# Kernel tuning notes

Hardware: AMD Instinct MI355X
Metric: run time of the kernel (lower is better)

## Reference

```python
import jax, jax.numpy as jnp
import numpy as np

DT = 0.1
ROUTER_BLOCKS = 64
REPEAT = 64
IN_SIZE = 2048
HIDDEN = 4096
NNZ_W = int(IN_SIZE * HIDDEN * 0.01)   # 83886
NNZ_R = int(HIDDEN * HIDDEN * 0.01)    # 167772
BATCH = 512


def sparse_linear(x, rows, cols, vals, bias, out_features):
    """Edge-list sparse matmul: out[b, cols[e]] += x[b, rows[e]] * vals[e].
    Equivalent to torch.addmm(bias, x, W_csr) with W built from COO (coalesce
    sums duplicates; scatter-add does the same)."""
    contrib = x[:, rows] * vals  # [B, nnz]
    out = jnp.zeros((x.shape[0], out_features), x.dtype).at[:, cols].add(contrib)
    return out + bias


def setup_inputs() -> dict:
    key = jax.random.key(0)
    ks = jax.random.split(key, 20)
    inp = {}
    inp["x"] = jax.random.normal(ks[0], (BATCH, IN_SIZE), jnp.float32)
    inp["h_prev"] = jax.random.normal(ks[1], (BATCH, HIDDEN), jnp.float32)
    inp["gate"] = jax.random.uniform(ks[2], (BATCH, 1), jnp.float32)
    # SparseLinear params (init scale 1/sqrt(in_features), bias zeros)
    inp["W_vals"] = jax.random.normal(ks[3], (NNZ_W,), jnp.float32) / np.sqrt(IN_SIZE).astype(np.float32)
    inp["W_bias"] = jnp.zeros((HIDDEN,), jnp.float32)
    inp["R_vals"] = jax.random.normal(ks[4], (NNZ_R,), jnp.float32) / np.sqrt(HIDDEN).astype(np.float32)
    inp["R_bias"] = jnp.zeros((HIDDEN,), jnp.float32)
    inp["P_vals"] = jax.random.normal(ks[5], (NNZ_R,), jnp.float32) / np.sqrt(HIDDEN).astype(np.float32)
    inp["P_bias"] = jnp.zeros((HIDDEN,), jnp.float32)
    inp["router_w"] = jax.random.normal(ks[6], (ROUTER_BLOCKS, IN_SIZE), jnp.float32) / np.sqrt(IN_SIZE).astype(np.float32)
    inp["router_b"] = jnp.zeros((ROUTER_BLOCKS,), jnp.float32)
    # tau ~ U(0.1, 0.5) per TAU_CONCEPT_RANGE
    inp["tau"] = jax.random.uniform(ks[7], (HIDDEN,), jnp.float32) * 0.4 + 0.1
    # edge lists (int constants)
    inp["W_rows"] = jax.random.randint(ks[8], (NNZ_W,), 0, IN_SIZE, jnp.int32)
    inp["W_cols"] = jax.random.randint(ks[9], (NNZ_W,), 0, HIDDEN, jnp.int32)
    inp["R_rows"] = jax.random.randint(ks[10], (NNZ_R,), 0, HIDDEN, jnp.int32)
    inp["R_cols"] = jax.random.randint(ks[11], (NNZ_R,), 0, HIDDEN, jnp.int32)
    inp["P_rows"] = jax.random.randint(ks[12], (NNZ_R,), 0, HIDDEN, jnp.int32)
    inp["P_cols"] = jax.random.randint(ks[13], (NNZ_R,), 0, HIDDEN, jnp.int32)
    return inp


def reference(x, h_prev, gate, W_vals, W_bias, R_vals, R_bias, P_vals, P_bias,
              router_w, router_b, tau, W_rows, W_cols, R_rows, R_cols, P_rows, P_cols):
    r_gate = jax.nn.sigmoid(x @ router_w.T + router_b)            # [B, 64]
    mask = jnp.repeat(r_gate, REPEAT, axis=1)[:, :HIDDEN]          # [B, hidden]
    sensory = sparse_linear(x, W_rows, W_cols, W_vals, W_bias, HIDDEN) * mask
    rec = sparse_linear(h_prev, R_rows, R_cols, R_vals, R_bias, HIDDEN)
    target = jnp.tanh(sensory + rec)
    h_new = h_prev + gate * (target - h_prev) * (DT / tau)
    pred = sparse_linear(h_new, P_rows, P_cols, P_vals, P_bias, HIDDEN)
    return (h_new, pred)
```

## Files before the change

### kernel.cpp

```cpp
#include <hip/hip_runtime.h>
#include <math.h>

namespace {

constexpr int B     = 512;
constexpr int IN    = 2048;
constexpr int HID   = 4096;
constexpr int NNZ_W = 83886;
constexpr int NNZ_R = 167772;
constexpr int NTOT  = NNZ_W + 2 * NNZ_R;
constexpr int NCOLS = 3 * HID;
constexpr int SLOT  = 128;
constexpr float DT  = 0.1f;

typedef float f4 __attribute__((ext_vector_type(4)));
typedef float f2 __attribute__((ext_vector_type(2)));

struct ushort4_t { unsigned short x, y, z, w; };

__device__ __forceinline__ float bf2f(unsigned short u) {
  return __uint_as_float((unsigned int)u << 16);
}
__device__ __forceinline__ unsigned short f2bf(float f) {
  unsigned int u = __float_as_uint(f);
  u += 0x7FFFu + ((u >> 16) & 1u);
  return (unsigned short)(u >> 16);
}

__global__ void prep_k(const float* __restrict__ x, unsigned short* __restrict__ xTb,
                       const float* __restrict__ h, float* __restrict__ hT,
                       unsigned short* __restrict__ hTb,
                       const float* __restrict__ rw, const float* __restrict__ rb,
                       float* __restrict__ rgT, int* __restrict__ cnt) {
  __shared__ float sh[4 * IN];
  const int blk = blockIdx.x;
  const int tid = threadIdx.x;

  if (blk < 768) {
    const bool isX = blk < 256;
    const float* src; int C, tb;
    if (isX) { src = x; C = IN;  tb = blk; }
    else     { src = h; C = HID; tb = blk - 256; }
    const int tx_n = C / 64;
    const int bx = (tb % tx_n) * 64;
    const int by = (tb / tx_n) * 64;
    const int tx = tid & 63;
    const int ty = tid >> 6;
    for (int i = ty; i < 64; i += 8)
      sh[i * 65 + tx] = src[(size_t)(by + i) * C + bx + tx];
    __syncthreads();
    for (int i = ty; i < 64; i += 8) {
      const float v = sh[tx * 65 + i];
      const size_t di = (size_t)(bx + i) * B + by + tx;
      if (isX) xTb[di] = f2bf(v);
      else     { hT[di] = v; hTb[di] = f2bf(v); }
    }
  } else if (blk < 896) {
    const int b0 = (blk - 768) * 4;
    for (int k = tid; k < 4 * IN; k += 512) sh[k] = x[(size_t)b0 * IN + k];
    __syncthreads();
    const int wave = tid >> 6;
    const int lane = tid & 63;
#pragma unroll
    for (int j = 0; j < 8; ++j) {
      const int o = wave * 8 + j;
      const float* w = rw + (size_t)o * IN;
      float s0 = 0.f, s1 = 0.f, s2 = 0.f, s3 = 0.f;
      for (int i = 0; i < IN / 64; ++i) {
        const float wv = w[lane + 64 * i];
        s0 += sh[0 * IN + lane + 64 * i] * wv;
        s1 += sh[1 * IN + lane + 64 * i] * wv;
        s2 += sh[2 * IN + lane + 64 * i] * wv;
        s3 += sh[3 * IN + lane + 64 * i] * wv;
      }
#pragma unroll
      for (int d = 1; d < 64; d <<= 1) {
        s0 += __shfl_xor(s0, d);
        s1 += __shfl_xor(s1, d);
        s2 += __shfl_xor(s2, d);
        s3 += __shfl_xor(s3, d);
      }
      if (lane == 0) {
        const float bias = rb[o];
        rgT[o * B + b0 + 0] = 1.f / (1.f + expf(-(s0 + bias)));
        rgT[o * B + b0 + 1] = 1.f / (1.f + expf(-(s1 + bias)));
        rgT[o * B + b0 + 2] = 1.f / (1.f + expf(-(s2 + bias)));
        rgT[o * B + b0 + 3] = 1.f / (1.f + expf(-(s3 + bias)));
      }
    }
  } else {
    const int i = (blk - 896) * 512 + tid;
    if (i < NCOLS) cnt[i] = 0;
  }
}

__global__ void slotscat_k(const int* __restrict__ Wc, const int* __restrict__ Rc,
                           const int* __restrict__ Pc, const int* __restrict__ Wr,
                           const int* __restrict__ Rr, const int* __restrict__ Pr,
                           const float* __restrict__ Wv, const float* __restrict__ Rv,
                           const float* __restrict__ Pv, int* __restrict__ cnt,
                           float2* __restrict__ packed) {
  const int i = blockIdx.x * blockDim.x + threadIdx.x;
  if (i >= NTOT) return;
  int gc, r; float v;
  if (i < NNZ_W)              { gc = Wc[i];                 r = Wr[i]; v = Wv[i]; }
  else if (i < NNZ_W + NNZ_R) { int j = i - NNZ_W;          gc = HID + Rc[j];     r = Rr[j]; v = Rv[j]; }
  else                        { int j = i - NNZ_W - NNZ_R; gc = 2 * HID + Pc[j]; r = Pr[j]; v = Pv[j]; }
  const int p = atomicAdd(&cnt[gc], 1);
  packed[(size_t)gc * SLOT + p] = make_float2(v, __int_as_float(r));
}

__device__ __forceinline__ f4 gather_col_bf(const unsigned short* __restrict__ srcb,
                                            const float2* __restrict__ packed,
                                            int gc, int n, int boff, float bias) {
  f4 acc; acc.x = bias; acc.y = bias; acc.z = bias; acc.w = bias;
  const f2* ep = (const f2*)(packed + (size_t)gc * SLOT);
  int i = 0;
  for (; i + 8 <= n; i += 8) {
    f2 e[8]; ushort4_t s[8];
#pragma unroll
    for (int j = 0; j < 8; ++j) e[j] = ep[i + j];
#pragma unroll
    for (int j = 0; j < 8; ++j)
      s[j] = *(const ushort4_t*)(srcb + (size_t)__float_as_int(e[j].y) * B + boff);
#pragma unroll
    for (int j = 0; j < 8; ++j) {
      acc.x += e[j].x * bf2f(s[j].x);
      acc.y += e[j].x * bf2f(s[j].y);
      acc.z += e[j].x * bf2f(s[j].z);
      acc.w += e[j].x * bf2f(s[j].w);
    }
  }
  for (; i < n; ++i) {
    const f2 e = ep[i];
    const ushort4_t s = *(const ushort4_t*)(srcb + (size_t)__float_as_int(e.y) * B + boff);
    acc.x += e.x * bf2f(s.x);
    acc.y += e.x * bf2f(s.y);
    acc.z += e.x * bf2f(s.z);
    acc.w += e.x * bf2f(s.w);
  }
  return acc;
}

__device__ __forceinline__ void col_chunk(int blk, int wave, int& c, int& boff,
                                          int lane, int& cgrp, int& chunk) {
  const int p = blk & 7;
  chunk = p >> 2;
  cgrp = ((p & 3) << 8) | (blk >> 3);
  c = cgrp * 4 + wave;
  boff = chunk * 256 + lane * 4;
}

__device__ __forceinline__ void store_tile_T(float* __restrict__ tile,
                                             const f4 v, int wave, int lane,
                                             int cgrp, int chunk,
                                             float* __restrict__ out) {
  ((f4*)tile)[wave * 64 + lane] = v;
  __syncthreads();
  const int t = threadIdx.x;
  f4 o;
  o.x = tile[0 * 256 + t];
  o.y = tile[1 * 256 + t];
  o.z = tile[2 * 256 + t];
  o.w = tile[3 * 256 + t];
  *(f4*)(out + (size_t)(chunk * 256 + t) * HID + cgrp * 4) = o;
}

__global__ void fused_gc_k(const unsigned short* __restrict__ xTb,
                           const unsigned short* __restrict__ hTb,
                           const float* __restrict__ hT,
                           const float2* __restrict__ packed, const int* __restrict__ cnt,
                           const float* __restrict__ rgT,
                           const float* __restrict__ gate, const float* __restrict__ tau,
                           const float* __restrict__ wb, const float* __restrict__ rb,
                           float* __restrict__ out_h, unsigned short* __restrict__ hnb) {
  __shared__ float tile[4 * 256];
  int c, boff, cgrp, chunk;
  const int wave = threadIdx.x >> 6, lane = threadIdx.x & 63;
  col_chunk(blockIdx.x, wave, c, boff, lane, cgrp, chunk);

  const f4 sens = gather_col_bf(xTb, packed, c, cnt[c], boff, wb[c]);
  const f4 rec  = gather_col_bf(hTb, packed, HID + c, cnt[HID + c], boff, rb[c]);

  const f4 m  = *(const f4*)(rgT + (size_t)(c >> 6) * B + boff);
  const f4 g  = *(const f4*)(gate + boff);
  const f4 hp = *(const f4*)(hT + (size_t)c * B + boff);
  const float k = DT / tau[c];
  f4 hn;
  hn.x = hp.x + g.x * (tanhf(sens.x * m.x + rec.x) - hp.x) * k;
  hn.y = hp.y + g.y * (tanhf(sens.y * m.y + rec.y) - hp.y) * k;
  hn.z = hp.z + g.z * (tanhf(sens.z * m.z + rec.z) - hp.z) * k;
  hn.w = hp.w + g.w * (tanhf(sens.w * m.w + rec.w) - hp.w) * k;

  ushort4_t hb;
  hb.x = f2bf(hn.x); hb.y = f2bf(hn.y); hb.z = f2bf(hn.z); hb.w = f2bf(hn.w);
  *(ushort4_t*)(hnb + (size_t)c * B + boff) = hb;

  store_tile_T(tile, hn, wave, lane, cgrp, chunk, out_h);
}

__global__ void pred_k(const unsigned short* __restrict__ hnb,
                       const float2* __restrict__ packed, const int* __restrict__ cnt,
                       const float* __restrict__ pb, float* __restrict__ out_p) {
  __shared__ float tile[4 * 256];
  int c, boff, cgrp, chunk;
  const int wave = threadIdx.x >> 6, lane = threadIdx.x & 63;
  col_chunk(blockIdx.x, wave, c, boff, lane, cgrp, chunk);
  const f4 p = gather_col_bf(hnb, packed, 2 * HID + c, cnt[2 * HID + c], boff, pb[c]);
  store_tile_T(tile, p, wave, lane, cgrp, chunk, out_p);
}

}

extern "C" void kernel_launch(void* const* d_in, const int* in_sizes, int n_in,
                              void* d_out, int out_size, void* d_ws, size_t ws_size,
                              hipStream_t stream) {
  const float* x        = (const float*)d_in[0];
  const float* h_prev   = (const float*)d_in[1];
  const float* gate     = (const float*)d_in[2];
  const float* W_vals   = (const float*)d_in[3];
  const float* W_bias   = (const float*)d_in[4];
  const float* R_vals   = (const float*)d_in[5];
  const float* R_bias   = (const float*)d_in[6];
  const float* P_vals   = (const float*)d_in[7];
  const float* P_bias   = (const float*)d_in[8];
  const float* router_w = (const float*)d_in[9];
  const float* router_b = (const float*)d_in[10];
  const float* tau      = (const float*)d_in[11];
  const int* W_rows = (const int*)d_in[12];
  const int* W_cols = (const int*)d_in[13];
  const int* R_rows = (const int*)d_in[14];
  const int* R_cols = (const int*)d_in[15];
  const int* P_rows = (const int*)d_in[16];
  const int* P_cols = (const int*)d_in[17];

  float* ws = (float*)d_ws;
  unsigned short* xTb = (unsigned short*)ws;
  float*  hT     = ws + (size_t)IN * B / 2;
  unsigned short* hTb = (unsigned short*)(hT + (size_t)HID * B);
  float*  rgT    = (float*)(hTb + (size_t)HID * B);
  unsigned short* hnb = (unsigned short*)(rgT + 64 * B);
  float2* packed = (float2*)(hnb + (size_t)HID * B);
  int*    cnt    = (int*)(packed + (size_t)NCOLS * SLOT);

  float* out_h = (float*)d_out;
  float* out_p = out_h + (size_t)B * HID;

  prep_k<<<920, 512, 0, stream>>>(x, xTb, h_prev, hT, hTb,
                                  router_w, router_b, rgT, cnt);

  slotscat_k<<<(NTOT + 255) / 256, 256, 0, stream>>>(W_cols, R_cols, P_cols,
                                                     W_rows, R_rows, P_rows,
                                                     W_vals, R_vals, P_vals,
                                                     cnt, packed);

  fused_gc_k<<<2048, 256, 0, stream>>>(xTb, hTb, hT, packed, cnt, rgT,
                                       gate, tau, W_bias, R_bias, out_h, hnb);

  pred_k<<<2048, 256, 0, stream>>>(hnb, packed, cnt, P_bias, out_p);
}
```

Before: 111.9 us.

## Have each wave cover the full batch with 8-wide bf16 gathers per lane

Each lane now processes 8 batch elements instead of 4, loading 16-byte bf16 vectors per gathered row. Each block covers four columns across the whole batch, which halves the block count and removes the batch-chunk swizzle. Every edge-list entry is now read once per column instead of once per batch chunk, which cuts redundant packed-edge loads and index latency. In exchange, register pressure rises, the shared tile doubles, and fewer blocks are available to hide gather latency.

```diff
diff --git a/kernel.cpp b/kernel.cpp
--- a/kernel.cpp
+++ b/kernel.cpp
@@ -15,8 +15,9 @@
 
 typedef float f4 __attribute__((ext_vector_type(4)));
 typedef float f2 __attribute__((ext_vector_type(2)));
-
-struct ushort4_t { unsigned short x, y, z, w; };
+typedef unsigned short us8 __attribute__((ext_vector_type(8)));
+
+struct f8 { f4 lo, hi; };
 
 __device__ __forceinline__ float bf2f(unsigned short u) {
   return __uint_as_float((unsigned int)u << 16);
@@ -110,60 +111,59 @@
   packed[(size_t)gc * SLOT + p] = make_float2(v, __int_as_float(r));
 }
 
-__device__ __forceinline__ f4 gather_col_bf(const unsigned short* __restrict__ srcb,
-                                            const float2* __restrict__ packed,
-                                            int gc, int n, int boff, float bias) {
-  f4 acc; acc.x = bias; acc.y = bias; acc.z = bias; acc.w = bias;
+__device__ __forceinline__ f8 gather_col_bf8(const unsigned short* __restrict__ srcb,
+                                             const float2* __restrict__ packed,
+                                             int gc, int n, int boff, float bias) {
+  f4 a0; a0.x = bias; a0.y = bias; a0.z = bias; a0.w = bias;
+  f4 a1 = a0;
   const f2* ep = (const f2*)(packed + (size_t)gc * SLOT);
   int i = 0;
   for (; i + 8 <= n; i += 8) {
-    f2 e[8]; ushort4_t s[8];
+    f2 e[8]; us8 s[8];
 #pragma unroll
     for (int j = 0; j < 8; ++j) e[j] = ep[i + j];
 #pragma unroll
     for (int j = 0; j < 8; ++j)
-      s[j] = *(const ushort4_t*)(srcb + (size_t)__float_as_int(e[j].y) * B + boff);
+      s[j] = *(const us8*)(srcb + (size_t)__float_as_int(e[j].y) * B + boff);
 #pragma unroll
     for (int j = 0; j < 8; ++j) {
-      acc.x += e[j].x * bf2f(s[j].x);
-      acc.y += e[j].x * bf2f(s[j].y);
-      acc.z += e[j].x * bf2f(s[j].z);
-      acc.w += e[j].x * bf2f(s[j].w);
+      const float v = e[j].x;
+      a0.x += v * bf2f(s[j][0]); a0.y += v * bf2f(s[j][1]);
+      a0.z += v * bf2f(s[j][2]); a0.w += v * bf2f(s[j][3]);
+      a1.x += v * bf2f(s[j][4]); a1.y += v * bf2f(s[j][5]);
+      a1.z += v * bf2f(s[j][6]); a1.w += v * bf2f(s[j][7]);
     }
   }
   for (; i < n; ++i) {
     const f2 e = ep[i];
-    const ushort4_t s = *(const ushort4_t*)(srcb + (size_t)__float_as_int(e.y) * B + boff);
-    acc.x += e.x * bf2f(s.x);
-    acc.y += e.x * bf2f(s.y);
-    acc.z += e.x * bf2f(s.z);
-    acc.w += e.x * bf2f(s.w);
-  }
-  return acc;
-}
-
-__device__ __forceinline__ void col_chunk(int blk, int wave, int& c, int& boff,
-                                          int lane, int& cgrp, int& chunk) {
-  const int p = blk & 7;
-  chunk = p >> 2;
-  cgrp = ((p & 3) << 8) | (blk >> 3);
-  c = cgrp * 4 + wave;
-  boff = chunk * 256 + lane * 4;
+    const us8 s = *(const us8*)(srcb + (size_t)__float_as_int(e.y) * B + boff);
+    const float v = e.x;
+    a0.x += v * bf2f(s[0]); a0.y += v * bf2f(s[1]);
+    a0.z += v * bf2f(s[2]); a0.w += v * bf2f(s[3]);
+    a1.x += v * bf2f(s[4]); a1.y += v * bf2f(s[5]);
+    a1.z += v * bf2f(s[6]); a1.w += v * bf2f(s[7]);
+  }
+  f8 r; r.lo = a0; r.hi = a1;
+  return r;
 }
 
 __device__ __forceinline__ void store_tile_T(float* __restrict__ tile,
-                                             const f4 v, int wave, int lane,
-                                             int cgrp, int chunk,
-                                             float* __restrict__ out) {
-  ((f4*)tile)[wave * 64 + lane] = v;
+                                             const f8 v, int wave, int lane,
+                                             int c0, float* __restrict__ out) {
+  ((f4*)tile)[wave * 128 + lane * 2 + 0] = v.lo;
+  ((f4*)tile)[wave * 128 + lane * 2 + 1] = v.hi;
   __syncthreads();
   const int t = threadIdx.x;
-  f4 o;
-  o.x = tile[0 * 256 + t];
-  o.y = tile[1 * 256 + t];
-  o.z = tile[2 * 256 + t];
-  o.w = tile[3 * 256 + t];
-  *(f4*)(out + (size_t)(chunk * 256 + t) * HID + cgrp * 4) = o;
+#pragma unroll
+  for (int r = 0; r < 2; ++r) {
+    const int b = r * 256 + t;
+    f4 o;
+    o.x = tile[0 * 512 + b];
+    o.y = tile[1 * 512 + b];
+    o.z = tile[2 * 512 + b];
+    o.w = tile[3 * 512 + b];
+    *(f4*)(out + (size_t)b * HID + c0) = o;
+  }
 }
 
 __global__ void fused_gc_k(const unsigned short* __restrict__ xTb,
@@ -174,40 +174,53 @@
                            const float* __restrict__ gate, const float* __restrict__ tau,
                            const float* __restrict__ wb, const float* __restrict__ rb,
                            float* __restrict__ out_h, unsigned short* __restrict__ hnb) {
-  __shared__ float tile[4 * 256];
-  int c, boff, cgrp, chunk;
+  __shared__ float tile[4 * 512];
   const int wave = threadIdx.x >> 6, lane = threadIdx.x & 63;
-  col_chunk(blockIdx.x, wave, c, boff, lane, cgrp, chunk);
-
-  const f4 sens = gather_col_bf(xTb, packed, c, cnt[c], boff, wb[c]);
-  const f4 rec  = gather_col_bf(hTb, packed, HID + c, cnt[HID + c], boff, rb[c]);
-
-  const f4 m  = *(const f4*)(rgT + (size_t)(c >> 6) * B + boff);
-  const f4 g  = *(const f4*)(gate + boff);
-  const f4 hp = *(const f4*)(hT + (size_t)c * B + boff);
+  const int c0 = blockIdx.x * 4;
+  const int c = c0 + wave;
+  const int boff = lane * 8;
+
+  const f8 sens = gather_col_bf8(xTb, packed, c, cnt[c], boff, wb[c]);
+  const f8 rec  = gather_col_bf8(hTb, packed, HID + c, cnt[HID + c], boff, rb[c]);
+
+  const float* rg = rgT + (size_t)(c >> 6) * B + boff;
+  const f4 m0 = *(const f4*)rg;
+  const f4 m1 = *(const f4*)(rg + 4);
+  const f4 g0 = *(const f4*)(gate + boff);
+  const f4 g1 = *(const f4*)(gate + boff + 4);
+  const float* hpp = hT + (size_t)c * B + boff;
+  const f4 hp0 = *(const f4*)hpp;
+  const f4 hp1 = *(const f4*)(hpp + 4);
   const float k = DT / tau[c];
-  f4 hn;
-  hn.x = hp.x + g.x * (tanhf(sens.x * m.x + rec.x) - hp.x) * k;
-  hn.y = hp.y + g.y * (tanhf(sens.y * m.y + rec.y) - hp.y) * k;
-  hn.z = hp.z + g.z * (tanhf(sens.z * m.z + rec.z) - hp.z) * k;
-  hn.w = hp.w + g.w * (tanhf(sens.w * m.w + rec.w) - hp.w) * k;
-
-  ushort4_t hb;
-  hb.x = f2bf(hn.x); hb.y = f2bf(hn.y); hb.z = f2bf(hn.z); hb.w = f2bf(hn.w);
-  *(ushort4_t*)(hnb + (size_t)c * B + boff) = hb;
-
-  store_tile_T(tile, hn, wave, lane, cgrp, chunk, out_h);
+
+  f8 hn;
+  hn.lo.x = hp0.x + g0.x * (tanhf(sens.lo.x * m0.x + rec.lo.x) - hp0.x) * k;
+  hn.lo.y = hp0.y + g0.y * (tanhf(sens.lo.y * m0.y + rec.lo.y) - hp0.y) * k;
+  hn.lo.z = hp0.z + g0.z * (tanhf(sens.lo.z * m0.z + rec.lo.z) - hp0.z) * k;
+  hn.lo.w = hp0.w + g0.w * (tanhf(sens.lo.w * m0.w + rec.lo.w) - hp0.w) * k;
+  hn.hi.x = hp1.x + g1.x * (tanhf(sens.hi.x * m1.x + rec.hi.x) - hp1.x) * k;
+  hn.hi.y = hp1.y + g1.y * (tanhf(sens.hi.y * m1.y + rec.hi.y) - hp1.y) * k;
+  hn.hi.z = hp1.z + g1.z * (tanhf(sens.hi.z * m1.z + rec.hi.z) - hp1.z) * k;
+  hn.hi.w = hp1.w + g1.w * (tanhf(sens.hi.w * m1.w + rec.hi.w) - hp1.w) * k;
+
+  us8 hb;
+  hb[0] = f2bf(hn.lo.x); hb[1] = f2bf(hn.lo.y); hb[2] = f2bf(hn.lo.z); hb[3] = f2bf(hn.lo.w);
+  hb[4] = f2bf(hn.hi.x); hb[5] = f2bf(hn.hi.y); hb[6] = f2bf(hn.hi.z); hb[7] = f2bf(hn.hi.w);
+  *(us8*)(hnb + (size_t)c * B + boff) = hb;
+
+  store_tile_T(tile, hn, wave, lane, c0, out_h);
 }
 
 __global__ void pred_k(const unsigned short* __restrict__ hnb,
                        const float2* __restrict__ packed, const int* __restrict__ cnt,
                        const float* __restrict__ pb, float* __restrict__ out_p) {
-  __shared__ float tile[4 * 256];
-  int c, boff, cgrp, chunk;
+  __shared__ float tile[4 * 512];
   const int wave = threadIdx.x >> 6, lane = threadIdx.x & 63;
-  col_chunk(blockIdx.x, wave, c, boff, lane, cgrp, chunk);
-  const f4 p = gather_col_bf(hnb, packed, 2 * HID + c, cnt[2 * HID + c], boff, pb[c]);
-  store_tile_T(tile, p, wave, lane, cgrp, chunk, out_p);
+  const int c0 = blockIdx.x * 4;
+  const int c = c0 + wave;
+  const int boff = lane * 8;
+  const f8 p = gather_col_bf8(hnb, packed, 2 * HID + c, cnt[2 * HID + c], boff, pb[c]);
+  store_tile_T(tile, p, wave, lane, c0, out_p);
 }
 
 }
@@ -254,8 +267,8 @@
                                                      W_vals, R_vals, P_vals,
                                                      cnt, packed);
 
-  fused_gc_k<<<2048, 256, 0, stream>>>(xTb, hTb, hT, packed, cnt, rgT,
-                                       gate, tau, W_bias, R_bias, out_h, hnb);
-
-  pred_k<<<2048, 256, 0, stream>>>(hnb, packed, cnt, P_bias, out_p);
-}
+  fused_gc_k<<<HID / 4, 256, 0, stream>>>(xTb, hTb, hT, packed, cnt, rgT,
+                                          gate, tau, W_bias, R_bias, out_h, hnb);
+
+  pred_k<<<HID / 4, 256, 0, stream>>>(hnb, packed, cnt, P_bias, out_p);
+}
```

Measured after the change: 98.89 us. 11.6% less time.
